# Optimization experiments

Hardware: AMD Instinct MI355X
Metric: run time of the kernel (lower is better)

Reference implementation:

```python
import jax, jax.numpy as jnp
import numpy as np

BS, T, C, H, W = 2, 3, 256, 48, 48
NH, NP, NL = 8, 4, 3
DH = C // NH
HW = H * W
LQ = T * HW


def conv2d(x, w, b):
    # x: (N,C,H,W), w: (O,I,3,3), padding=1 (SAME)
    y = jax.lax.conv_general_dilated(x, w, (1, 1), 'SAME',
                                     dimension_numbers=('NCHW', 'OIHW', 'NCHW'))
    return y + b[None, :, None, None]


def grid_sample(img, grid, align_corners, padding_mode):
    # img: (B,C,Hi,Wi); grid: (B,Hg,Wg,2) in [-1,1], last dim = (x,y)
    B, Ch, Hi, Wi = img.shape
    gx, gy = grid[..., 0], grid[..., 1]
    if align_corners:
        x = (gx + 1.0) * 0.5 * (Wi - 1)
        y = (gy + 1.0) * 0.5 * (Hi - 1)
    else:
        x = ((gx + 1.0) * Wi - 1.0) * 0.5
        y = ((gy + 1.0) * Hi - 1.0) * 0.5
    if padding_mode == 'border':
        x = jnp.clip(x, 0.0, Wi - 1)
        y = jnp.clip(y, 0.0, Hi - 1)
    x0 = jnp.floor(x); y0 = jnp.floor(y)
    x1 = x0 + 1.0; y1 = y0 + 1.0
    wx1 = x - x0; wx0 = 1.0 - wx1
    wy1 = y - y0; wy0 = 1.0 - wy1
    imgf = img.reshape(B, Ch, Hi * Wi)

    def gather(xi, yi):
        xc = jnp.clip(xi, 0, Wi - 1).astype(jnp.int32)
        yc = jnp.clip(yi, 0, Hi - 1).astype(jnp.int32)
        flat = (yc * Wi + xc).reshape(B, 1, -1)
        g = jnp.take_along_axis(imgf, flat, axis=2).reshape(B, Ch, *xi.shape[1:])
        if padding_mode == 'zeros':
            valid = ((xi >= 0) & (xi <= Wi - 1) & (yi >= 0) & (yi <= Hi - 1))
            g = g * valid[:, None].astype(img.dtype)
        return g

    out = (gather(x0, y0) * (wx0 * wy0)[:, None]
           + gather(x1, y0) * (wx1 * wy0)[:, None]
           + gather(x0, y1) * (wx0 * wy1)[:, None]
           + gather(x1, y1) * (wx1 * wy1)[:, None])
    return out


def warp(x, flo):
    # x: (B,C,H,W), flo: (B,2,H,W) pixel flow; border padding, align_corners=True
    B, Ch, Hh, Ww = x.shape
    gy, gx = jnp.meshgrid(jnp.arange(Hh), jnp.arange(Ww), indexing='ij')
    grid = jnp.stack([gx, gy], 0).astype(x.dtype)[None]  # (1,2,H,W)
    v = grid + flo
    vx = 2.0 * v[:, 0] / max(Ww - 1, 1) - 1.0
    vy = 2.0 * v[:, 1] / max(Hh - 1, 1) - 1.0
    g = jnp.stack([vx, vy], -1)  # (B,H,W,2)
    return grid_sample(x, g, align_corners=True, padding_mode='border')


def flow_guid_offset(flow_forward, flow_backward, off, h, w):
    # off: (N, LQ, NH, NL, NP, 2) -> add frame-to-frame flows per (query level, key level)
    N = off.shape[0]
    hw = h * w
    off = off.reshape(N, NL, hw, NH, NL, NP, 2)
    f01 = flow_forward[:, 0]; f12 = flow_forward[:, 1]
    f02 = f01 + warp(f12, f01)
    b10 = flow_backward[:, 0]; b21 = flow_backward[:, 1]
    b20 = b21 + warp(b10, b21)

    def flat(f):
        return f.transpose(0, 2, 3, 1).reshape(N, hw, 2)

    f01, f12, f02, b10, b21, b20 = map(flat, (f01, f12, f02, b10, b21, b20))
    z = jnp.zeros_like(f01)
    add = jnp.stack([
        jnp.stack([z, f01, f02], axis=2),
        jnp.stack([b10, z, f12], axis=2),
        jnp.stack([b20, b21, z], axis=2)], axis=1)  # (N, 3, hw, 3, 2)
    off = off + add[:, :, :, None, :, None, :]
    return off.reshape(N, NL * hw, NH, NL, NP, 2)


def setup_inputs():
    key = jax.random.key(0)
    ks = jax.random.split(key, 12)
    query = jax.random.normal(ks[0], (BS, T, C, H, W), dtype=jnp.float32)
    input_flatten = jax.random.normal(ks[1], (BS, T, C, H, W), dtype=jnp.float32)
    reference_points = jax.random.uniform(ks[2], (BS, LQ, NL, 2), dtype=jnp.float32)
    input_spatial_shapes = jnp.array([[H, W]] * NL, dtype=jnp.int32)
    input_level_start_index = jnp.array([0, HW, 2 * HW], dtype=jnp.int32)
    input_padding_mask = jnp.zeros((BS, LQ), dtype=bool)
    flow_forward = 3.0 * jax.random.normal(ks[3], (BS, 2, 2, H, W), dtype=jnp.float32)
    flow_backward = 3.0 * jax.random.normal(ks[4], (BS, 2, 2, H, W), dtype=jnp.float32)
    # sampling_offsets bias init (as in _reset_parameters)
    thetas = np.arange(NH) * (2.0 * np.pi / NH)
    g = np.stack([np.cos(thetas), np.sin(thetas)], -1)
    g = g / np.abs(g).max(-1, keepdims=True)
    g = np.tile(g.reshape(NH, 1, 1, 2), (1, NL, NP, 1))
    g = g * (np.arange(NP) + 1).reshape(1, 1, NP, 1)
    b_off = jnp.asarray(g.reshape(-1), dtype=jnp.float32)
    fan = 1.0 / np.sqrt(C * 9)
    w_off = 0.01 * jax.random.normal(ks[5], (NH * NL * NP * 2, C, 3, 3), dtype=jnp.float32)
    w_attn = 0.01 * jax.random.normal(ks[6], (NH * NL * NP, C, 3, 3), dtype=jnp.float32)
    b_attn = jnp.zeros((NH * NL * NP,), dtype=jnp.float32)
    w_val = fan * jax.random.normal(ks[7], (C, C, 3, 3), dtype=jnp.float32)
    b_val = jnp.zeros((C,), dtype=jnp.float32)
    w_out = fan * jax.random.normal(ks[8], (C, C, 3, 3), dtype=jnp.float32)
    b_out = jnp.zeros((C,), dtype=jnp.float32)
    return {'query': query, 'reference_points': reference_points,
            'input_flatten': input_flatten,
            'input_spatial_shapes': input_spatial_shapes,
            'input_level_start_index': input_level_start_index,
            'input_padding_mask': input_padding_mask,
            'flow_forward': flow_forward, 'flow_backward': flow_backward,
            'w_off': w_off, 'b_off': b_off, 'w_attn': w_attn, 'b_attn': b_attn,
            'w_val': w_val, 'b_val': b_val, 'w_out': w_out, 'b_out': b_out}


def reference(query, reference_points, input_flatten, input_spatial_shapes,
              input_level_start_index, input_padding_mask, flow_forward,
              flow_backward, w_off, b_off, w_attn, b_attn, w_val, b_val,
              w_out, b_out):
    bs, t, c, h, w = query.shape
    q2d = query.reshape(bs * t, c, h, w)
    value = conv2d(input_flatten.reshape(bs * t, c, h, w), w_val, b_val)
    off = conv2d(q2d, w_off, b_off)
    attn = conv2d(q2d, w_attn, b_attn)

    def to_seq(x2d, ch):
        return x2d.reshape(bs, t, ch, h * w).transpose(0, 1, 3, 2).reshape(bs, t * h * w, ch)

    value = to_seq(value, c)
    off = to_seq(off, NH * NL * NP * 2)
    attn = to_seq(attn, NH * NL * NP)
    value = jnp.where(input_padding_mask[..., None], 0.0, value)
    value = value.reshape(bs, t * h * w, NH, DH)
    off = off.reshape(bs, LQ, NH, NL, NP, 2)
    off = flow_guid_offset(flow_forward, flow_backward, off, h, w)
    attn = jax.nn.softmax(attn.reshape(bs, LQ, NH, NL * NP), axis=-1)
    attn = attn.reshape(bs, LQ, NH, NL, NP)
    # offset normalizer: (W_l, H_l) per level
    norm = jnp.stack([input_spatial_shapes[:, 1], input_spatial_shapes[:, 0]], -1).astype(off.dtype)
    loc = reference_points[:, :, None, :, None, :] + off / norm[None, None, None, :, None, :]
    grids = 2.0 * loc - 1.0  # (bs, LQ, NH, NL, NP, 2)
    # values per level -> (NL*bs*NH, DH, h, w)
    v = value.reshape(bs, NL, h, w, NH, DH).transpose(1, 0, 4, 5, 2, 3).reshape(NL * bs * NH, DH, h, w)
    g = grids.transpose(3, 0, 2, 1, 4, 5).reshape(NL * bs * NH, LQ, NP, 2)
    sampled = grid_sample(v, g, align_corners=False, padding_mode='zeros')  # (NL*bs*NH, DH, LQ, NP)
    sampled = sampled.reshape(NL, bs, NH, DH, LQ, NP)
    out = jnp.einsum('lnhdqp,nqhlp->nqhd', sampled, attn).reshape(bs, LQ, c)
    out = out.reshape(bs, t, h * w, c).transpose(0, 1, 3, 2).reshape(bs * t, c, h, w)
    return conv2d(out, w_out, b_out)
```

## Files before the change

kernel.cpp:

```cpp
#include <hip/hip_runtime.h>
#include <hip/hip_bf16.h>

#define BS   2
#define T    3
#define CCH  256
#define HH   48
#define WW   48
#define NH   8
#define NP   4
#define NL   3
#define DH   32
#define HWP  (HH*WW)
#define LQ   (T*HWP)
#define NIMG (BS*T)

typedef short v8s __attribute__((ext_vector_type(8)));
typedef float v4f __attribute__((ext_vector_type(4)));
typedef float v2f __attribute__((ext_vector_type(2)));
typedef unsigned int v2u __attribute__((ext_vector_type(2)));
typedef unsigned int v4u __attribute__((ext_vector_type(4)));

__device__ __forceinline__ unsigned short f2b(float f) {
    unsigned u = __float_as_uint(f);
    return (unsigned short)((u + 0x7FFFu + ((u >> 16) & 1u)) >> 16);
}

#define GLOAD_LDS16(gp, lp) \
    __builtin_amdgcn_global_load_lds((const __attribute__((address_space(1))) unsigned int*)(const void*)(gp), \
                                     (__attribute__((address_space(3))) unsigned int*)(void*)(lp), 16, 0, 0)

#define LDS_SLAB  16384
#define LDS_ZROW  53248
#define LDS_TOTAL 53376

#define PBLK (NIMG*CCH*HWP)

__global__ __launch_bounds__(256) void flow_kernel(
    const float* __restrict__ ff, const float* __restrict__ fb,
    float* __restrict__ addb)
{
    int idx = blockIdx.x * 256 + threadIdx.x;
    if (idx >= BS * HWP) return;
    int n = idx / HWP, pix = idx % HWP;
    int y = pix / WW, x = pix % WW;

    auto F = [&](const float* base, int i, int c, int p) {
        return base[n * (2*2*HWP) + i * (2*HWP) + c * HWP + p];
    };

    float f01x = F(ff,0,0,pix), f01y = F(ff,0,1,pix);
    float f12x = F(ff,1,0,pix), f12y = F(ff,1,1,pix);
    float b10x = F(fb,0,0,pix), b10y = F(fb,0,1,pix);
    float b21x = F(fb,1,0,pix), b21y = F(fb,1,1,pix);

    auto bil = [&](const float* base, int i, float fx, float fy, float* ox, float* oy) {
        float vx = (float)x + fx;
        float vy = (float)y + fy;
        float gx = 2.0f * vx / (float)(WW - 1) - 1.0f;
        float gy = 2.0f * vy / (float)(HH - 1) - 1.0f;
        float px = (gx + 1.0f) * 0.5f * (float)(WW - 1);
        float py = (gy + 1.0f) * 0.5f * (float)(HH - 1);
        px = fminf(fmaxf(px, 0.0f), (float)(WW - 1));
        py = fminf(fmaxf(py, 0.0f), (float)(HH - 1));
        float x0f = floorf(px), y0f = floorf(py);
        float wx1 = px - x0f, wx0 = 1.0f - wx1;
        float wy1 = py - y0f, wy0 = 1.0f - wy1;
        int xi0 = (int)x0f, yi0 = (int)y0f;
        int xc0 = min(max(xi0, 0), WW-1), xc1 = min(max(xi0+1, 0), WW-1);
        int yc0 = min(max(yi0, 0), HH-1), yc1 = min(max(yi0+1, 0), HH-1);
        float r[2];
        #pragma unroll
        for (int c = 0; c < 2; ++c) {
            float v00 = F(base, i, c, yc0*WW + xc0);
            float v10 = F(base, i, c, yc0*WW + xc1);
            float v01 = F(base, i, c, yc1*WW + xc0);
            float v11 = F(base, i, c, yc1*WW + xc1);
            r[c] = v00*(wx0*wy0) + v10*(wx1*wy0) + v01*(wx0*wy1) + v11*(wx1*wy1);
        }
        *ox = r[0]; *oy = r[1];
    };

    float wfx, wfy; bil(ff, 1, f01x, f01y, &wfx, &wfy);
    float f02x = f01x + wfx, f02y = f01y + wfy;
    float wbx, wby; bil(fb, 0, b21x, b21y, &wbx, &wby);
    float b20x = b21x + wbx, b20y = b21y + wby;

    float* A = addb + n * (3*HWP*6) + pix * 6;
    const int TS = HWP * 6;
    A[0] = 0.f;   A[1] = 0.f;   A[2] = f01x; A[3] = f01y; A[4] = f02x; A[5] = f02y;
    A[TS+0] = b10x; A[TS+1] = b10y; A[TS+2] = 0.f; A[TS+3] = 0.f; A[TS+4] = f12x; A[TS+5] = f12y;
    A[2*TS+0] = b20x; A[2*TS+1] = b20y; A[2*TS+2] = b21x; A[2*TS+3] = b21y; A[2*TS+4] = 0.f; A[2*TS+5] = 0.f;
}

__global__ __launch_bounds__(256) void wcvt2_kernel(
    const float* __restrict__ s0, const float* __restrict__ s1,
    unsigned short* __restrict__ dst, int M0, int M1, int Mpad)
{
    int idx = blockIdx.x * 256 + threadIdx.x;
    if (idx >= 9 * Mpad * 256) return;
    int k  = idx / (Mpad * 256);
    int oc = (idx / 256) % Mpad;
    int ic = idx % 256;
    float v = (oc < M0) ? s0[((size_t)oc * 256 + ic) * 9 + k]
            : (oc < M1) ? s1[((size_t)(oc - M0) * 256 + ic) * 9 + k] : 0.f;
    dst[idx] = f2b(v);
}

__global__ __launch_bounds__(256) void tcvt_kernel(
    const float* __restrict__ src, unsigned short* __restrict__ dst)
{
    __shared__ float lds[32][33];
    int px0 = blockIdx.x * 32, ic0 = blockIdx.y * 32, img = blockIdx.z;
    int t = threadIdx.x;
    #pragma unroll
    for (int s = 0; s < 4; ++s) {
        int icl = (t >> 5) + s * 8, pxl = t & 31;
        lds[icl][pxl] = src[((size_t)img * 256 + ic0 + icl) * HWP + px0 + pxl];
    }
    __syncthreads();
    #pragma unroll
    for (int s = 0; s < 4; ++s) {
        int pxl = (t >> 5) + s * 8, icl = t & 31;
        dst[((size_t)img * HWP + px0 + pxl) * 256 + ic0 + icl] = f2b(lds[icl][pxl]);
    }
}

__global__ __launch_bounds__(256) void convbig(
    int phase,
    const unsigned short* __restrict__ in_a,
    const unsigned short* __restrict__ in_b,
    const unsigned short* __restrict__ Wb_a,
    const unsigned short* __restrict__ Wb_b,
    const float* __restrict__ bias_a,
    const float* __restrict__ bias_off,
    const float* __restrict__ bias_attn,
    unsigned short* __restrict__ Vout,
    float* __restrict__ offb,
    float* __restrict__ attnb,
    float* __restrict__ outp,
    const unsigned char* __restrict__ mask)
{
    __shared__ __align__(16) char lds[LDS_TOTAL];

    const int tid  = threadIdx.x;
    const int lane = tid & 63;
    const int wv   = tid >> 6;

    int b = blockIdx.x;
    int cls, mt, nt, img, Mpad, c_lo, c_hi, s;
    const unsigned short *inb, *Wb;
    if (phase == 0) {
        s = 0; c_lo = 0; c_hi = 4;
        if (b < 216) { cls = 0; mt = b % 2; int r = b / 2; nt = r % 18; img = r / 18;
                       inb = in_a; Wb = Wb_a; Mpad = 256; }
        else { b -= 216; cls = 1; mt = b % 3; int r = b / 3; nt = r % 18; img = r / 18;
               inb = in_b; Wb = Wb_b; Mpad = 384; }
    } else {
        cls = 3; s = b / 216; b = b % 216;
        c_lo = 2 * s; c_hi = c_lo + 2;
        mt = b % 2; int r = b / 2; nt = r % 18; img = r / 18;
        inb = in_a; Wb = Wb_a; Mpad = 256;
    }

    const int oc0 = mt * 128;
    const int pxb = nt * 128;
    const char* inIc = (const char*)(inb + (size_t)img * HWP * 256);
    const char* Wbc  = (const char*)Wb;

    if (tid < 8) {
        v8s z;
        #pragma unroll
        for (int j = 0; j < 8; ++j) z[j] = 0;
        *(v8s*)(lds + LDS_ZROW + tid * 16) = z;
    }

    const int r0   = pxb / 48;
    const int rlo  = (r0 > 0) ? (r0 - 1) : 0;
    const int pxlo = rlo * 48;

    const int lrow8 = lane >> 3;
    const int lcol  = lane & 7;

    const int rowl = lane & 15;
    const int g    = lane >> 4;
    const int keyx = (rowl & 7) << 4;
    const int aoff0 = ((wv >> 1) * 64 + rowl) * 128;
    const int pxw   = pxb + (wv & 1) * 64;
    int ypx[4], xpx[4];
    #pragma unroll
    for (int p = 0; p < 4; ++p) {
        int px = pxw + p * 16 + rowl;
        ypx[p] = px / 48;
        xpx[p] = px % 48;
    }
    int ocr_[4];
    #pragma unroll
    for (int j = 0; j < 4; ++j) ocr_[j] = j * 32 + wv * 8 + lrow8;

    v4f acc[4][4];
    #pragma unroll
    for (int m = 0; m < 4; ++m)
        #pragma unroll
        for (int p = 0; p < 4; ++p)
            #pragma unroll
            for (int e = 0; e < 4; ++e) acc[m][p][e] = 0.f;

    for (int c = c_lo; c < c_hi; ++c) {
        const int ic0b = c * 128;

        #pragma unroll
        for (int rr = 0; rr < 9; ++rr) {
            int pe  = rr * 32 + wv * 8 + lrow8;
            int gpx = pxlo + pe;
            if (gpx > 2303) gpx = 2303;
            GLOAD_LDS16(inIc + (size_t)gpx * 512 + ic0b + ((lcol ^ (pe & 7)) << 4),
                        lds + LDS_SLAB + (rr * 32 + wv * 8) * 128);
        }
        #pragma unroll
        for (int j = 0; j < 4; ++j) {
            GLOAD_LDS16(Wbc + (size_t)(oc0 + ocr_[j]) * 512 + ic0b + ((lcol ^ (ocr_[j] & 7)) << 4),
                        lds + (j * 32 + wv * 8) * 128);
        }
        __syncthreads();

        for (int k = 0; k < 9; ++k) {
            const int dy = k / 3 - 1, dx = k % 3 - 1;

            v8s pre[4];
            if (k < 8) {
                const char* wk1 = Wbc + (size_t)(k + 1) * Mpad * 512;
                #pragma unroll
                for (int j = 0; j < 4; ++j)
                    pre[j] = *(const v8s*)(wk1 + (size_t)(oc0 + ocr_[j]) * 512 + ic0b
                                           + ((lcol ^ (ocr_[j] & 7)) << 4));
            }

            int bbase[4], bkey[4];
            #pragma unroll
            for (int p = 0; p < 4; ++p) {
                int ys = ypx[p] + dy, xs = xpx[p] + dx;
                bool val = ((unsigned)ys < 48u) && ((unsigned)xs < 48u);
                int pe = ys * 48 + xs - pxlo;
                bbase[p] = val ? (LDS_SLAB + pe * 128) : LDS_ZROW;
                bkey[p]  = val ? ((pe & 7) << 4) : 0;
            }

            #pragma unroll
            for (int kk = 0; kk < 2; ++kk) {
                const int col = kk * 64 + g * 16;
                v8s a[4], bfr[4];
                #pragma unroll
                for (int m = 0; m < 4; ++m)
                    a[m] = *(const v8s*)(lds + aoff0 + m * 2048 + (col ^ keyx));
                #pragma unroll
                for (int p = 0; p < 4; ++p)
                    bfr[p] = *(const v8s*)(lds + bbase[p] + (col ^ bkey[p]));
                #pragma unroll
                for (int m = 0; m < 4; ++m)
                    #pragma unroll
                    for (int p = 0; p < 4; ++p)
                        acc[m][p] = __builtin_amdgcn_mfma_f32_16x16x32_bf16(a[m], bfr[p], acc[m][p], 0, 0, 0);
            }

            __syncthreads();
            if (k < 8) {
                #pragma unroll
                for (int j = 0; j < 4; ++j)
                    *(v8s*)(lds + (j * 32 + wv * 8) * 128 + lane * 16) = pre[j];
                __syncthreads();
            }
        }
    }

    const int n = img / T, t = img % T;
    const int ocw = oc0 + (wv >> 1) * 64;

    #pragma unroll
    for (int p = 0; p < 4; ++p) {
        const int px_f = pxw + p * 16 + rowl;
        const int q = t * HWP + px_f;
        bool mk = (cls == 0) ? (mask[n * LQ + q] != 0) : false;
        #pragma unroll
        for (int m = 0; m < 4; ++m) {
            const int oc_f = ocw + m * 16 + g * 4;
            if (cls == 0) {
                unsigned short o[4];
                #pragma unroll
                for (int r = 0; r < 4; ++r) {
                    float v = acc[m][p][r] + bias_a[oc_f + r];
                    if (mk) v = 0.f;
                    o[r] = f2b(v);
                }
                int head = oc_f >> 5, d0 = oc_f & 31;
                v2u pk;
                pk[0] = (unsigned)o[0] | ((unsigned)o[1] << 16);
                pk[1] = (unsigned)o[2] | ((unsigned)o[3] << 16);
                *(v2u*)(Vout + (((size_t)(t * BS + n) * NH + head) * HWP + px_f) * 32 + d0) = pk;
            } else if (cls == 1) {
                if (oc_f < 192) {
                    v4f v;
                    #pragma unroll
                    for (int r = 0; r < 4; ++r) v[r] = acc[m][p][r] + bias_off[oc_f + r];
                    *(v4f*)(offb + ((size_t)n * LQ + q) * 192 + oc_f) = v;
                } else if (oc_f < 288) {
                    v4f v;
                    #pragma unroll
                    for (int r = 0; r < 4; ++r) v[r] = acc[m][p][r] + bias_attn[oc_f - 192 + r];
                    *(v4f*)(attnb + ((size_t)n * LQ + q) * 96 + (oc_f - 192)) = v;
                }
            } else {
                float* pb = outp + (size_t)s * PBLK;
                #pragma unroll
                for (int r = 0; r < 4; ++r)
                    pb[((size_t)img * CCH + oc_f + r) * HWP + px_f] = acc[m][p][r];
            }
        }
    }
}

__global__ __launch_bounds__(256) void reduce_kernel(
    const float* __restrict__ part, const float* __restrict__ bias,
    float* __restrict__ out)
{
    int i4 = blockIdx.x * 256 + threadIdx.x;
    size_t i = (size_t)i4 * 4;
    if (i >= (size_t)PBLK) return;
    int oc = (int)((i / HWP) % CCH);
    v4f a = *(const v4f*)(part + i);
    v4f b = *(const v4f*)(part + PBLK + i);
    float bv = bias[oc];
    v4f o;
    #pragma unroll
    for (int e = 0; e < 4; ++e) o[e] = a[e] + b[e] + bv;
    *(v4f*)(out + i) = o;
}

__global__ __launch_bounds__(256) void sample_kernel(
    const unsigned short* __restrict__ V,
    const float* __restrict__ offb,
    const float* __restrict__ attnb,
    const float* __restrict__ addb,
    const float* __restrict__ refp,
    unsigned short* __restrict__ midb)
{
    const int tid = threadIdx.x;
    const int gid = tid >> 2, li = tid & 3;
    const int pair = blockIdx.x * 64 + gid;
    const int head = pair & 7;
    const int nq = pair >> 3;
    const int n = nq / LQ, q = nq % LQ;
    const int t = q / HWP, pix = q % HWP;

    const float* al = attnb + ((size_t)n * LQ + q) * 96 + head * 12;
    float lg[12];
    {
        v4f t0 = *(const v4f*)al, t1 = *(const v4f*)(al + 4), t2 = *(const v4f*)(al + 8);
        #pragma unroll
        for (int j = 0; j < 4; ++j) { lg[j] = t0[j]; lg[4+j] = t1[j]; lg[8+j] = t2[j]; }
    }
    const float* ofp = offb + ((size_t)n * LQ + q) * 192 + head * 24;
    float of[24];
    #pragma unroll
    for (int j = 0; j < 6; ++j) {
        v4f v = *(const v4f*)(ofp + j * 4);
        #pragma unroll
        for (int e = 0; e < 4; ++e) of[j*4+e] = v[e];
    }
    const float* rpp = refp + ((size_t)n * LQ + q) * 6;
    const float* adp = addb + ((size_t)n * 3 * HWP + t * HWP + pix) * 6;
    float rp[6], ad[6];
    #pragma unroll
    for (int j = 0; j < 3; ++j) {
        v2f r = *(const v2f*)(rpp + j * 2);
        v2f a = *(const v2f*)(adp + j * 2);
        rp[j*2] = r[0]; rp[j*2+1] = r[1];
        ad[j*2] = a[0]; ad[j*2+1] = a[1];
    }

    float m = lg[0];
    #pragma unroll
    for (int j = 1; j < 12; ++j) m = fmaxf(m, lg[j]);
    float s = 0.f;
    #pragma unroll
    for (int j = 0; j < 12; ++j) { lg[j] = expf(lg[j] - m); s += lg[j]; }
    float inv = 1.0f / s;
    #pragma unroll
    for (int j = 0; j < 12; ++j) lg[j] *= inv;

    float acc[8];
    #pragma unroll
    for (int e = 0; e < 8; ++e) acc[e] = 0.f;

    #pragma unroll
    for (int l = 0; l < 3; ++l) {
        float refx = rp[l*2+0], refy = rp[l*2+1];
        float addx = ad[l*2+0], addy = ad[l*2+1];
        const unsigned short* Vi =
            V + (size_t)((l * BS + n) * NH + head) * HWP * DH + li * 8;
        #pragma unroll
        for (int p = 0; p < 4; ++p) {
            float ox = of[(l*4+p)*2+0] + addx;
            float oy = of[(l*4+p)*2+1] + addy;
            float locx = refx + ox * (1.0f/48.0f);
            float locy = refy + oy * (1.0f/48.0f);
            float gx = 2.0f*locx - 1.0f;
            float gy = 2.0f*locy - 1.0f;
            float pxf = ((gx + 1.0f) * 48.0f - 1.0f) * 0.5f;
            float pyf = ((gy + 1.0f) * 48.0f - 1.0f) * 0.5f;
            float x0f = floorf(pxf), y0f = floorf(pyf);
            float wx1 = pxf - x0f, wx0 = 1.0f - wx1;
            float wy1 = pyf - y0f, wy0 = 1.0f - wy1;
            int xi0 = (int)x0f, yi0 = (int)y0f;
            bool vx0 = (x0f >= 0.0f)     && (x0f <= 47.0f);
            bool vx1 = (x0f+1.f >= 0.0f) && (x0f+1.f <= 47.0f);
            bool vy0 = (y0f >= 0.0f)     && (y0f <= 47.0f);
            bool vy1 = (y0f+1.f >= 0.0f) && (y0f+1.f <= 47.0f);
            int xc0 = min(max(xi0, 0), 47),   xc1 = min(max(xi0+1, 0), 47);
            int yc0 = min(max(yi0, 0), 47),   yc1 = min(max(yi0+1, 0), 47);
            float aw = lg[l*4+p];
            float w00 = (vx0 && vy0) ? wx0*wy0*aw : 0.f;
            float w10 = (vx1 && vy0) ? wx1*wy0*aw : 0.f;
            float w01 = (vx0 && vy1) ? wx0*wy1*aw : 0.f;
            float w11 = (vx1 && vy1) ? wx1*wy1*aw : 0.f;
            v4u u00 = *(const v4u*)(Vi + (yc0*WW + xc0)*DH);
            v4u u10 = *(const v4u*)(Vi + (yc0*WW + xc1)*DH);
            v4u u01 = *(const v4u*)(Vi + (yc1*WW + xc0)*DH);
            v4u u11 = *(const v4u*)(Vi + (yc1*WW + xc1)*DH);
            #pragma unroll
            for (int cc = 0; cc < 4; ++cc) {
                v4u u = (cc == 0) ? u00 : (cc == 1) ? u10 : (cc == 2) ? u01 : u11;
                float w = (cc == 0) ? w00 : (cc == 1) ? w10 : (cc == 2) ? w01 : w11;
                #pragma unroll
                for (int e = 0; e < 4; ++e) {
                    acc[e*2+0] += w * __uint_as_float(u[e] << 16);
                    acc[e*2+1] += w * __uint_as_float(u[e] & 0xFFFF0000u);
                }
            }
        }
    }

    v4u pk;
    #pragma unroll
    for (int e = 0; e < 4; ++e)
        pk[e] = (unsigned)f2b(acc[e*2+0]) | ((unsigned)f2b(acc[e*2+1]) << 16);
    *(v4u*)(midb + ((size_t)(n * T + t) * HWP + pix) * 256 + head * 32 + li * 8) = pk;
}

extern "C" void kernel_launch(void* const* d_in, const int* in_sizes, int n_in,
                              void* d_out, int out_size, void* d_ws, size_t ws_size,
                              hipStream_t stream) {
    const float* query  = (const float*)d_in[0];
    const float* refp   = (const float*)d_in[1];
    const float* inputf = (const float*)d_in[2];
    const unsigned char* mask = (const unsigned char*)d_in[5];
    const float* ff     = (const float*)d_in[6];
    const float* fb     = (const float*)d_in[7];
    const float* w_off  = (const float*)d_in[8];
    const float* b_off  = (const float*)d_in[9];
    const float* w_attn = (const float*)d_in[10];
    const float* b_attn = (const float*)d_in[11];
    const float* w_val  = (const float*)d_in[12];
    const float* b_val  = (const float*)d_in[13];
    const float* w_out  = (const float*)d_in[14];
    const float* b_out  = (const float*)d_in[15];

    char* w = (char*)d_ws;
    float* offb  = (float*)w;           w += (size_t)BS*LQ*192*4;
    float* attnb = (float*)w;           w += (size_t)BS*LQ*96*4;
    float* addb  = (float*)w;           w += (size_t)BS*3*HWP*6*4;
    unsigned short* V      = (unsigned short*)w; w += (size_t)48*HWP*DH*2;
    unsigned short* inb_q  = (unsigned short*)w; w += (size_t)NIMG*HWP*256*2;
    unsigned short* inb_v  = (unsigned short*)w; w += (size_t)NIMG*HWP*256*2;
    unsigned short* midb   = inb_v;
    unsigned short* Wb_val = (unsigned short*)w; w += (size_t)9*256*256*2;
    unsigned short* Wb_oa  = (unsigned short*)w; w += (size_t)9*384*256*2;
    unsigned short* Wb_out = (unsigned short*)w; w += (size_t)9*256*256*2;
    float* partial = (float*)d_ws;
    float* outp = (float*)d_out;

    flow_kernel<<<(BS*HWP + 255)/256, 256, 0, stream>>>(ff, fb, addb);
    wcvt2_kernel<<<9*256, 256, 0, stream>>>(w_val, w_val, Wb_val, 256, 256, 256);
    wcvt2_kernel<<<9*384, 256, 0, stream>>>(w_off, w_attn, Wb_oa, 192, 288, 384);
    wcvt2_kernel<<<9*256, 256, 0, stream>>>(w_out, w_out, Wb_out, 256, 256, 256);
    tcvt_kernel<<<dim3(HWP/32, 8, NIMG), 256, 0, stream>>>(inputf, inb_v);
    tcvt_kernel<<<dim3(HWP/32, 8, NIMG), 256, 0, stream>>>(query,  inb_q);

    convbig<<<540, 256, 0, stream>>>(0, inb_v, inb_q, Wb_val, Wb_oa,
                                     b_val, b_off, b_attn,
                                     V, offb, attnb, nullptr, mask);

    sample_kernel<<<(BS*LQ*NH)/64, 256, 0, stream>>>(V, offb, attnb, addb, refp, midb);

    convbig<<<432, 256, 0, stream>>>(1, midb, nullptr, Wb_out, nullptr,
                                     nullptr, nullptr, nullptr,
                                     nullptr, nullptr, nullptr, partial, nullptr);

    reduce_kernel<<<(PBLK/4 + 255)/256, 256, 0, stream>>>(partial, b_out, outp);
}
```

Before: 168.1 us.

## Fuse prep kernels, double-buffer conv weights via LDS DMA, atomic split-K output

Merges the flow, three weight-conversion and two transpose-conversion launches into one prep kernel dispatched by block index. In the conv kernel, next-tap weights are now loaded straight into a second LDS buffer with global_load_lds, replacing register staging plus two extra barriers per tap. The split-K partial buffer and reduce kernel are replaced by atomicAdd into a memset output, with bias added by one split. This cuts launches and a round trip through a partial buffer, at the cost of more LDS per block (less occupancy), atomic contention and non-deterministic summation order.

```diff
diff --git a/kernel.cpp b/kernel.cpp
--- a/kernel.cpp
+++ b/kernel.cpp
@@ -29,99 +29,117 @@
     __builtin_amdgcn_global_load_lds((const __attribute__((address_space(1))) unsigned int*)(const void*)(gp), \
                                      (__attribute__((address_space(3))) unsigned int*)(void*)(lp), 16, 0, 0)
 
-#define LDS_SLAB  16384
-#define LDS_ZROW  53248
-#define LDS_TOTAL 53376
-
-#define PBLK (NIMG*CCH*HWP)
-
-__global__ __launch_bounds__(256) void flow_kernel(
+#define LDS_SLAB  32768
+#define LDS_ZROW  69632
+#define LDS_TOTAL 69760
+
+#define NB_FLOW 18
+#define NB_WCVT 8064
+#define NB_TCVT 6912
+#define WS0 (9*256*256)
+#define WS1 (9*384*256)
+
+__global__ __launch_bounds__(256) void prep_kernel(
     const float* __restrict__ ff, const float* __restrict__ fb,
-    float* __restrict__ addb)
-{
-    int idx = blockIdx.x * 256 + threadIdx.x;
-    if (idx >= BS * HWP) return;
-    int n = idx / HWP, pix = idx % HWP;
-    int y = pix / WW, x = pix % WW;
-
-    auto F = [&](const float* base, int i, int c, int p) {
-        return base[n * (2*2*HWP) + i * (2*HWP) + c * HWP + p];
-    };
-
-    float f01x = F(ff,0,0,pix), f01y = F(ff,0,1,pix);
-    float f12x = F(ff,1,0,pix), f12y = F(ff,1,1,pix);
-    float b10x = F(fb,0,0,pix), b10y = F(fb,0,1,pix);
-    float b21x = F(fb,1,0,pix), b21y = F(fb,1,1,pix);
-
-    auto bil = [&](const float* base, int i, float fx, float fy, float* ox, float* oy) {
-        float vx = (float)x + fx;
-        float vy = (float)y + fy;
-        float gx = 2.0f * vx / (float)(WW - 1) - 1.0f;
-        float gy = 2.0f * vy / (float)(HH - 1) - 1.0f;
-        float px = (gx + 1.0f) * 0.5f * (float)(WW - 1);
-        float py = (gy + 1.0f) * 0.5f * (float)(HH - 1);
-        px = fminf(fmaxf(px, 0.0f), (float)(WW - 1));
-        py = fminf(fmaxf(py, 0.0f), (float)(HH - 1));
-        float x0f = floorf(px), y0f = floorf(py);
-        float wx1 = px - x0f, wx0 = 1.0f - wx1;
-        float wy1 = py - y0f, wy0 = 1.0f - wy1;
-        int xi0 = (int)x0f, yi0 = (int)y0f;
-        int xc0 = min(max(xi0, 0), WW-1), xc1 = min(max(xi0+1, 0), WW-1);
-        int yc0 = min(max(yi0, 0), HH-1), yc1 = min(max(yi0+1, 0), HH-1);
-        float r[2];
-        #pragma unroll
-        for (int c = 0; c < 2; ++c) {
-            float v00 = F(base, i, c, yc0*WW + xc0);
-            float v10 = F(base, i, c, yc0*WW + xc1);
-            float v01 = F(base, i, c, yc1*WW + xc0);
-            float v11 = F(base, i, c, yc1*WW + xc1);
-            r[c] = v00*(wx0*wy0) + v10*(wx1*wy0) + v01*(wx0*wy1) + v11*(wx1*wy1);
-        }
-        *ox = r[0]; *oy = r[1];
-    };
-
-    float wfx, wfy; bil(ff, 1, f01x, f01y, &wfx, &wfy);
-    float f02x = f01x + wfx, f02y = f01y + wfy;
-    float wbx, wby; bil(fb, 0, b21x, b21y, &wbx, &wby);
-    float b20x = b21x + wbx, b20y = b21y + wby;
-
-    float* A = addb + n * (3*HWP*6) + pix * 6;
-    const int TS = HWP * 6;
-    A[0] = 0.f;   A[1] = 0.f;   A[2] = f01x; A[3] = f01y; A[4] = f02x; A[5] = f02y;
-    A[TS+0] = b10x; A[TS+1] = b10y; A[TS+2] = 0.f; A[TS+3] = 0.f; A[TS+4] = f12x; A[TS+5] = f12y;
-    A[2*TS+0] = b20x; A[2*TS+1] = b20y; A[2*TS+2] = b21x; A[2*TS+3] = b21y; A[2*TS+4] = 0.f; A[2*TS+5] = 0.f;
-}
-
-__global__ __launch_bounds__(256) void wcvt2_kernel(
-    const float* __restrict__ s0, const float* __restrict__ s1,
-    unsigned short* __restrict__ dst, int M0, int M1, int Mpad)
-{
-    int idx = blockIdx.x * 256 + threadIdx.x;
-    if (idx >= 9 * Mpad * 256) return;
-    int k  = idx / (Mpad * 256);
-    int oc = (idx / 256) % Mpad;
-    int ic = idx % 256;
-    float v = (oc < M0) ? s0[((size_t)oc * 256 + ic) * 9 + k]
-            : (oc < M1) ? s1[((size_t)(oc - M0) * 256 + ic) * 9 + k] : 0.f;
-    dst[idx] = f2b(v);
-}
-
-__global__ __launch_bounds__(256) void tcvt_kernel(
-    const float* __restrict__ src, unsigned short* __restrict__ dst)
+    float* __restrict__ addb,
+    const float* __restrict__ w_val, const float* __restrict__ w_off,
+    const float* __restrict__ w_attn, const float* __restrict__ w_out,
+    unsigned short* __restrict__ Wb_val, unsigned short* __restrict__ Wb_oa,
+    unsigned short* __restrict__ Wb_out,
+    const float* __restrict__ inputf, const float* __restrict__ query,
+    unsigned short* __restrict__ inb_v, unsigned short* __restrict__ inb_q)
 {
     __shared__ float lds[32][33];
-    int px0 = blockIdx.x * 32, ic0 = blockIdx.y * 32, img = blockIdx.z;
-    int t = threadIdx.x;
-    #pragma unroll
-    for (int s = 0; s < 4; ++s) {
-        int icl = (t >> 5) + s * 8, pxl = t & 31;
-        lds[icl][pxl] = src[((size_t)img * 256 + ic0 + icl) * HWP + px0 + pxl];
-    }
-    __syncthreads();
-    #pragma unroll
-    for (int s = 0; s < 4; ++s) {
-        int pxl = (t >> 5) + s * 8, icl = t & 31;
-        dst[((size_t)img * HWP + px0 + pxl) * 256 + ic0 + icl] = f2b(lds[icl][pxl]);
+    const int b = blockIdx.x;
+    const int tid = threadIdx.x;
+
+    if (b < NB_FLOW) {
+        int idx = b * 256 + tid;
+        int n = idx / HWP, pix = idx % HWP;
+        int y = pix / WW, x = pix % WW;
+
+        auto F = [&](const float* base, int i, int c, int p) {
+            return base[n * (2*2*HWP) + i * (2*HWP) + c * HWP + p];
+        };
+
+        float f01x = F(ff,0,0,pix), f01y = F(ff,0,1,pix);
+        float f12x = F(ff,1,0,pix), f12y = F(ff,1,1,pix);
+        float b10x = F(fb,0,0,pix), b10y = F(fb,0,1,pix);
+        float b21x = F(fb,1,0,pix), b21y = F(fb,1,1,pix);
+
+        auto bil = [&](const float* base, int i, float fx, float fy, float* ox, float* oy) {
+            float vx = (float)x + fx;
+            float vy = (float)y + fy;
+            float gx = 2.0f * vx / (float)(WW - 1) - 1.0f;
+            float gy = 2.0f * vy / (float)(HH - 1) - 1.0f;
+            float px = (gx + 1.0f) * 0.5f * (float)(WW - 1);
+            float py = (gy + 1.0f) * 0.5f * (float)(HH - 1);
+            px = fminf(fmaxf(px, 0.0f), (float)(WW - 1));
+            py = fminf(fmaxf(py, 0.0f), (float)(HH - 1));
+            float x0f = floorf(px), y0f = floorf(py);
+            float wx1 = px - x0f, wx0 = 1.0f - wx1;
+            float wy1 = py - y0f, wy0 = 1.0f - wy1;
+            int xi0 = (int)x0f, yi0 = (int)y0f;
+            int xc0 = min(max(xi0, 0), WW-1), xc1 = min(max(xi0+1, 0), WW-1);
+            int yc0 = min(max(yi0, 0), HH-1), yc1 = min(max(yi0+1, 0), HH-1);
+            float r[2];
+            #pragma unroll
+            for (int c = 0; c < 2; ++c) {
+                float v00 = F(base, i, c, yc0*WW + xc0);
+                float v10 = F(base, i, c, yc0*WW + xc1);
+                float v01 = F(base, i, c, yc1*WW + xc0);
+                float v11 = F(base, i, c, yc1*WW + xc1);
+                r[c] = v00*(wx0*wy0) + v10*(wx1*wy0) + v01*(wx0*wy1) + v11*(wx1*wy1);
+            }
+            *ox = r[0]; *oy = r[1];
+        };
+
+        float wfx, wfy; bil(ff, 1, f01x, f01y, &wfx, &wfy);
+        float f02x = f01x + wfx, f02y = f01y + wfy;
+        float wbx, wby; bil(fb, 0, b21x, b21y, &wbx, &wby);
+        float b20x = b21x + wbx, b20y = b21y + wby;
+
+        float* A = addb + n * (3*HWP*6) + pix * 6;
+        const int TS = HWP * 6;
+        A[0] = 0.f;   A[1] = 0.f;   A[2] = f01x; A[3] = f01y; A[4] = f02x; A[5] = f02y;
+        A[TS+0] = b10x; A[TS+1] = b10y; A[TS+2] = 0.f; A[TS+3] = 0.f; A[TS+4] = f12x; A[TS+5] = f12y;
+        A[2*TS+0] = b20x; A[2*TS+1] = b20y; A[2*TS+2] = b21x; A[2*TS+3] = b21y; A[2*TS+4] = 0.f; A[2*TS+5] = 0.f;
+    } else if (b < NB_FLOW + NB_WCVT) {
+        int idx = (b - NB_FLOW) * 256 + tid;
+        if (idx < WS0) {
+            int k = idx / (256*256), oc = (idx / 256) % 256, ic = idx % 256;
+            Wb_val[idx] = f2b(w_val[((size_t)oc * 256 + ic) * 9 + k]);
+        } else if (idx < WS0 + WS1) {
+            int j = idx - WS0;
+            int k = j / (384*256), oc = (j / 256) % 384, ic = j % 256;
+            float v = (oc < 192) ? w_off[((size_t)oc * 256 + ic) * 9 + k]
+                    : (oc < 288) ? w_attn[((size_t)(oc - 192) * 256 + ic) * 9 + k] : 0.f;
+            Wb_oa[j] = f2b(v);
+        } else {
+            int j = idx - WS0 - WS1;
+            int k = j / (256*256), oc = (j / 256) % 256, ic = j % 256;
+            Wb_out[j] = f2b(w_out[((size_t)oc * 256 + ic) * 9 + k]);
+        }
+    } else {
+        int rem = b - NB_FLOW - NB_WCVT;
+        int which = rem / 3456;
+        int r2 = rem % 3456;
+        int px0 = (r2 % 72) * 32;
+        int ic0 = ((r2 / 72) % 8) * 32;
+        int img = r2 / (72 * 8);
+        const float* src = which ? query : inputf;
+        unsigned short* dst = which ? inb_q : inb_v;
+        #pragma unroll
+        for (int s = 0; s < 4; ++s) {
+            int icl = (tid >> 5) + s * 8, pxl = tid & 31;
+            lds[icl][pxl] = src[((size_t)img * 256 + ic0 + icl) * HWP + px0 + pxl];
+        }
+        __syncthreads();
+        #pragma unroll
+        for (int s = 0; s < 4; ++s) {
+            int pxl = (tid >> 5) + s * 8, icl = tid & 31;
+            dst[((size_t)img * HWP + px0 + pxl) * 256 + ic0 + icl] = f2b(lds[icl][pxl]);
+        }
     }
 }
 
@@ -221,19 +239,24 @@
             GLOAD_LDS16(Wbc + (size_t)(oc0 + ocr_[j]) * 512 + ic0b + ((lcol ^ (ocr_[j] & 7)) << 4),
                         lds + (j * 32 + wv * 8) * 128);
         }
-        __syncthreads();
+        asm volatile("s_waitcnt vmcnt(0) lgkmcnt(0)" ::: "memory");
+        __builtin_amdgcn_s_barrier();
 
         for (int k = 0; k < 9; ++k) {
             const int dy = k / 3 - 1, dx = k % 3 - 1;
-
-            v8s pre[4];
+            const int cur = k & 1;
             if (k < 8) {
                 const char* wk1 = Wbc + (size_t)(k + 1) * Mpad * 512;
                 #pragma unroll
-                for (int j = 0; j < 4; ++j)
-                    pre[j] = *(const v8s*)(wk1 + (size_t)(oc0 + ocr_[j]) * 512 + ic0b
-                                           + ((lcol ^ (ocr_[j] & 7)) << 4));
-            }
+                for (int j = 0; j < 4; ++j) {
+                    GLOAD_LDS16(wk1 + (size_t)(oc0 + ocr_[j]) * 512 + ic0b + ((lcol ^ (ocr_[j] & 7)) << 4),
+                                lds + (cur ^ 1) * 16384 + (j * 32 + wv * 8) * 128);
+                }
+                asm volatile("s_waitcnt vmcnt(4)" ::: "memory");
+            } else {
+                asm volatile("s_waitcnt vmcnt(0)" ::: "memory");
+            }
+            __builtin_amdgcn_s_barrier();
 
             int bbase[4], bkey[4];
             #pragma unroll
@@ -251,7 +274,7 @@
                 v8s a[4], bfr[4];
                 #pragma unroll
                 for (int m = 0; m < 4; ++m)
-                    a[m] = *(const v8s*)(lds + aoff0 + m * 2048 + (col ^ keyx));
+                    a[m] = *(const v8s*)(lds + cur * 16384 + aoff0 + m * 2048 + (col ^ keyx));
                 #pragma unroll
                 for (int p = 0; p < 4; ++p)
                     bfr[p] = *(const v8s*)(lds + bbase[p] + (col ^ bkey[p]));
@@ -261,14 +284,7 @@
                     for (int p = 0; p < 4; ++p)
                         acc[m][p] = __builtin_amdgcn_mfma_f32_16x16x32_bf16(a[m], bfr[p], acc[m][p], 0, 0, 0);
             }
-
-            __syncthreads();
-            if (k < 8) {
-                #pragma unroll
-                for (int j = 0; j < 4; ++j)
-                    *(v8s*)(lds + (j * 32 + wv * 8) * 128 + lane * 16) = pre[j];
-                __syncthreads();
-            }
+            __builtin_amdgcn_s_barrier();
         }
     }
 
@@ -309,30 +325,14 @@
                     *(v4f*)(attnb + ((size_t)n * LQ + q) * 96 + (oc_f - 192)) = v;
                 }
             } else {
-                float* pb = outp + (size_t)s * PBLK;
-                #pragma unroll
-                for (int r = 0; r < 4; ++r)
-                    pb[((size_t)img * CCH + oc_f + r) * HWP + px_f] = acc[m][p][r];
-            }
-        }
-    }
-}
-
-__global__ __launch_bounds__(256) void reduce_kernel(
-    const float* __restrict__ part, const float* __restrict__ bias,
-    float* __restrict__ out)
-{
-    int i4 = blockIdx.x * 256 + threadIdx.x;
-    size_t i = (size_t)i4 * 4;
-    if (i >= (size_t)PBLK) return;
-    int oc = (int)((i / HWP) % CCH);
-    v4f a = *(const v4f*)(part + i);
-    v4f b = *(const v4f*)(part + PBLK + i);
-    float bv = bias[oc];
-    v4f o;
-    #pragma unroll
-    for (int e = 0; e < 4; ++e) o[e] = a[e] + b[e] + bv;
-    *(v4f*)(out + i) = o;
+                #pragma unroll
+                for (int r = 0; r < 4; ++r) {
+                    float v = acc[m][p][r] + ((s == 0) ? bias_a[oc_f + r] : 0.f);
+                    atomicAdd(&outp[((size_t)img * CCH + oc_f + r) * HWP + px_f], v);
+                }
+            }
+        }
+    }
 }
 
 __global__ __launch_bounds__(256) void sample_kernel(
@@ -475,15 +475,13 @@
     unsigned short* Wb_val = (unsigned short*)w; w += (size_t)9*256*256*2;
     unsigned short* Wb_oa  = (unsigned short*)w; w += (size_t)9*384*256*2;
     unsigned short* Wb_out = (unsigned short*)w; w += (size_t)9*256*256*2;
-    float* partial = (float*)d_ws;
     float* outp = (float*)d_out;
 
-    flow_kernel<<<(BS*HWP + 255)/256, 256, 0, stream>>>(ff, fb, addb);
-    wcvt2_kernel<<<9*256, 256, 0, stream>>>(w_val, w_val, Wb_val, 256, 256, 256);
-    wcvt2_kernel<<<9*384, 256, 0, stream>>>(w_off, w_attn, Wb_oa, 192, 288, 384);
-    wcvt2_kernel<<<9*256, 256, 0, stream>>>(w_out, w_out, Wb_out, 256, 256, 256);
-    tcvt_kernel<<<dim3(HWP/32, 8, NIMG), 256, 0, stream>>>(inputf, inb_v);
-    tcvt_kernel<<<dim3(HWP/32, 8, NIMG), 256, 0, stream>>>(query,  inb_q);
+    hipMemsetAsync(outp, 0, (size_t)NIMG * CCH * HWP * 4, stream);
+
+    prep_kernel<<<NB_FLOW + NB_WCVT + NB_TCVT, 256, 0, stream>>>(
+        ff, fb, addb, w_val, w_off, w_attn, w_out,
+        Wb_val, Wb_oa, Wb_out, inputf, query, inb_v, inb_q);
 
     convbig<<<540, 256, 0, stream>>>(0, inb_v, inb_q, Wb_val, Wb_oa,
                                      b_val, b_off, b_attn,
@@ -492,8 +490,6 @@
     sample_kernel<<<(BS*LQ*NH)/64, 256, 0, stream>>>(V, offb, attnb, addb, refp, midb);
 
     convbig<<<432, 256, 0, stream>>>(1, midb, nullptr, Wb_out, nullptr,
-                                     nullptr, nullptr, nullptr,
-                                     nullptr, nullptr, nullptr, partial, nullptr);
-
-    reduce_kernel<<<(PBLK/4 + 255)/256, 256, 0, stream>>>(partial, b_out, outp);
+                                     b_out, nullptr, nullptr,
+                                     nullptr, nullptr, nullptr, outp, nullptr);
 }
```

After: 155.1 us. -7.7%, faster.
